# Performance work log

Measured on AMD Instinct MI355X. Metric: run time of the kernel, lower is better.

## Reference

```python
import jax, jax.numpy as jnp
import numpy as np

C = 16          # number of classes
LAM = 25.0      # lambda_param (invariance)
MU = 25.0       # mu_param (variance)
NU = 1.0        # nu_param (covariance)
ALPHA = 50.0    # alpha_param (class-discriminative margin & weight)
EPS = 1e-4


def setup_inputs() -> dict:
    key = jax.random.key(0)
    k1, k2, k3 = jax.random.split(key, 3)
    N, D = 32768, 256
    z_a = jax.random.normal(k1, (N, D), dtype=jnp.float32)
    z_b = jax.random.normal(k2, (N, D), dtype=jnp.float32)
    labels = jax.random.randint(k3, (N,), 0, C)
    return {"z_a": z_a, "z_b": z_b, "labels": labels}


def _class_stats(x, labels):
    # counts [C], mean [C,D], unbiased var [C,D] via one segmented pass
    ones = jnp.ones(x.shape[0], x.dtype)
    counts = jax.ops.segment_sum(ones, labels, num_segments=C)
    s = jax.ops.segment_sum(x, labels, num_segments=C)
    sq = jax.ops.segment_sum(x * x, labels, num_segments=C)
    mean = s / counts[:, None]
    var = (sq - counts[:, None] * mean * mean) / (counts[:, None] - 1.0)
    return counts, mean, var


def _variance_loss(var):
    # mean over classes of mean_D relu(1 - std); D equal per class -> global mean
    std = jnp.sqrt(var + EPS)
    return jnp.mean(jax.nn.relu(1.0 - std))


def _covariance_loss(x, labels, counts, mean):
    D = x.shape[1]
    e = x - mean[labels]  # centered per class

    def per_class(c):
        w = (labels == c).astype(x.dtype)
        em = e * w[:, None]
        cov = em.T @ em / (counts[c] - 1.0)  # [D, D]
        off = (cov * cov).sum() - (jnp.diagonal(cov) ** 2).sum()
        return off / D

    return jnp.mean(jax.lax.map(per_class, jnp.arange(C)))


def _class_disc_loss(mean_a, mean_b):
    m = 0.5 * (mean_a + mean_b)               # [C, D]
    diff = m[:, None, :] - m[None, :, :]      # [C, C, D]
    d2 = jnp.sum(diff * diff, axis=-1)        # [C, C]
    mask = jnp.triu(jnp.ones((C, C), bool), 1)
    dist = jnp.sqrt(jnp.where(mask, d2, 1.0))  # safe sqrt off-mask
    pen = jnp.where(mask, jax.nn.relu(ALPHA - dist) ** 2, 0.0)
    npairs = C * (C - 1) // 2
    return pen.sum() / npairs


def reference(z_a, z_b, labels):
    inv_loss = jnp.mean((z_a - z_b) ** 2)
    ca, ma, va = _class_stats(z_a, labels)
    cb, mb, vb = _class_stats(z_b, labels)
    var_loss = 0.5 * (_variance_loss(va) + _variance_loss(vb))
    cov_loss = 0.5 * (_covariance_loss(z_a, labels, ca, ma)
                      + _covariance_loss(z_b, labels, cb, mb))
    class_loss = _class_disc_loss(ma, mb)
    return LAM * inv_loss + MU * var_loss + NU * cov_loss + ALPHA * class_loss
```

## Files before the change

kernel.cpp:

```cpp
#include <hip/hip_runtime.h>
#include <math.h>

#define N_ROWS 32768
#define D 256
#define C 16

#define WS_SUMS_A 0
#define WS_SQ_A   4096
#define WS_SUMS_B 8192
#define WS_SQ_B   12288
#define WS_INV    16384
#define WS_COV    16385
#define WS_COUNTS 16392
#define WS_CURSOR 16408
#define WS_POFFP  16424
#define WS_EOFF   16448
#define WS_INVP   16512
#define WS_COVP   17024
#define WS_PERM   17920
#define WS_ZERO_FLOATS 16408

#define WS_PSUM   50688
#define WS_HPART  181760
#define WS_GPART2 189952
#define GP_TILE2  4096
#define NTASK     10
#define NSPLIT    8
#define K2        2
#define GP_PER_SPLIT2 (NTASK * C * 2 * GP_TILE2)
#define RIDX_CAP  1024
#define NEED_A ((size_t)(WS_GPART2 + NSPLIT * GP_PER_SPLIT2) * 4)

typedef __attribute__((ext_vector_type(8))) __bf16 bf16x8;
typedef __attribute__((ext_vector_type(16))) float f32x16;

__device__ inline unsigned bf16_rne(float f) {
    unsigned u = __float_as_uint(f);
    return (u + 0x7fffu + ((u >> 16) & 1u)) >> 16;
}
__device__ inline unsigned pack_bf16(float lo, float hi) {
    return bf16_rne(lo) | (bf16_rne(hi) << 16);
}
__device__ inline int img_base4(int c, int kd) {
    return c * 20 + ((kd + ((c >> 1) & 12)) & 12);
}
__device__ inline int img_base2(int c, int kd) {
    return c * 20 + ((kd + ((c >> 1) & 12)) & 14);
}
__device__ inline void task_rc(int w, int& r, int& c) {
    if (w < 4)      { r = 0; c = w; }
    else if (w < 7) { r = 1; c = w - 3; }
    else if (w < 9) { r = 2; c = w - 5; }
    else            { r = 3; c = 3; }
}


__global__ __launch_bounds__(256) void k_pre(const float* __restrict__ za,
                                             const float* __restrict__ zb,
                                             const int* __restrict__ labels,
                                             int* __restrict__ hpart,
                                             float* __restrict__ ws) {
    const int t = threadIdx.x;
    const int b = blockIdx.x;
    __shared__ int h[C];
    if (t < C) h[t] = 0;
    __syncthreads();
    if (t < 64) atomicAdd(&h[labels[b * 64 + t]], 1);

    const int base = b * 4096 + t;
    float acc = 0.f;
    #pragma unroll
    for (int k = 0; k < 16; ++k) {
        const int i = base + k * 256;
        const float4 a = ((const float4*)za)[i];
        const float4 v = ((const float4*)zb)[i];
        const float dx = a.x - v.x, dy = a.y - v.y;
        const float dz = a.z - v.z, dw = a.w - v.w;
        acc += dx * dx + dy * dy + dz * dz + dw * dw;
    }
    for (int o = 32; o > 0; o >>= 1) acc += __shfl_down(acc, o, 64);
    __shared__ float red[4];
    if ((t & 63) == 0) red[t >> 6] = acc;
    __syncthreads();
    if (t < C) hpart[b * C + t] = h[t];
    if (t == 0) ws[WS_INVP + b] = red[0] + red[1] + red[2] + red[3];
}

__global__ __launch_bounds__(512) void k_scatter2(const int* __restrict__ labels,
                                                  const int* __restrict__ hpart,
                                                  int* __restrict__ counts,
                                                  int* __restrict__ poffp,
                                                  int* __restrict__ eoffp,
                                                  int* __restrict__ perm) {
    const int t = threadIdx.x;
    const int B = blockIdx.x;
    __shared__ int lh[C];
    __shared__ int tot[32][C];
    __shared__ int pre[32][C];
    __shared__ int ccnt[C], cpre[C], ceoff[C];
    const int i = B * 512 + t;
    const int lab = labels[i];
    if (t < C) lh[t] = 0;
    const int c = t & 15, seg = t >> 4;
    {
        int tt = 0, pp = 0;
        const int plo = seg * 16, pcut = B * 8;
        #pragma unroll
        for (int p = plo; p < plo + 16; ++p) {
            const int v = hpart[p * C + c];
            tt += v;
            if (p < pcut) pp += v;
        }
        tot[seg][c] = tt;
        pre[seg][c] = pp;
    }
    __syncthreads();
    const int lr = atomicAdd(&lh[lab], 1);
    if (t < C) {
        int s1 = 0, s2 = 0;
        #pragma unroll
        for (int g = 0; g < 32; ++g) { s1 += tot[g][t]; s2 += pre[g][t]; }
        ccnt[t] = s1;
        cpre[t] = s2;
    }
    __syncthreads();
    if (t == 0) {
        int off = 0, po = 0;
        for (int cc = 0; cc < C; ++cc) {
            ceoff[cc] = off;
            if (B == 0) { eoffp[cc] = off; poffp[cc] = po; counts[cc] = ccnt[cc]; }
            off += ccnt[cc];
            po += (ccnt[cc] + 31) >> 5;
        }
        if (B == 0) { eoffp[C] = off; poffp[C] = po; }
    }
    __syncthreads();
    perm[ceoff[lab] + cpre[lab] + lr] = i;
}

__global__ __launch_bounds__(640) void k_gram6(const float* __restrict__ za,
                                               const float* __restrict__ zb,
                                               const int* __restrict__ perm,
                                               const int* __restrict__ counts,
                                               const int* __restrict__ poffp,
                                               const int* __restrict__ eoffp,
                                               float* __restrict__ ws) {
    const int t = threadIdx.x;
    const int split = blockIdx.x;
    const int cls = blockIdx.y, inp = blockIdx.z;
    const float* X = inp ? zb : za;
    const int cnt = counts[cls];
    const int eoff = eoffp[cls];
    const int nsteps = poffp[cls + 1] - poffp[cls];
    const int chunk = (nsteps + NSPLIT - 1) / NSPLIT;
    const int sb = split * chunk;
    const int se = min(sb + chunk, nsteps);

    __shared__ __align__(16) unsigned img[2][5120];
    __shared__ float sstats[512];
    __shared__ int ridx[RIDX_CAP];

    for (int i = t; i < 512; i += 640) sstats[i] = 0.f;
    const int nl = (se > sb) ? (se - sb) * 32 : 0;
    for (int i = t; i < nl && i < RIDX_CAP; i += 640) {
        const int gr = sb * 32 + i;
        ridx[i] = (gr < cnt) ? perm[eoff + gr] : -1;
    }
    __syncthreads();

    auto rowidx = [&](int li) -> int {
        if (li < RIDX_CAP) return ridx[li];
        const int gr = sb * 32 + li;
        return (gr < cnt) ? perm[eoff + gr] : -1;
    };

    const int lane = t & 63, w = t >> 6;
    const int cg = lane & 31, q = lane >> 5;
    int tr, tc;
    task_rc(w, tr, tc);
    const bool stg = (t < 512);

    const int lc = 4 * (t & 63);
    const int kp0 = 2 * ((t >> 6) & 7);

    f32x16 acc[2][2];
    #pragma unroll
    for (int i = 0; i < 2; ++i)
        #pragma unroll
        for (int j = 0; j < 2; ++j) acc[i][j] = 0.0f;

    float s1r[4] = {0.f, 0.f, 0.f, 0.f};
    float s2r[4] = {0.f, 0.f, 0.f, 0.f};
    float4 f0[2], f1[2];

    auto load_regs = [&](int s) {
        #pragma unroll
        for (int it = 0; it < 2; ++it) {
            const int li = (s - sb) * 32 + 2 * (kp0 + it);
            const int r0 = rowidx(li), r1 = rowidx(li + 1);
            f0[it] = (r0 >= 0) ? *(const float4*)(X + (size_t)r0 * D + lc)
                               : make_float4(0.f, 0.f, 0.f, 0.f);
            f1[it] = (r1 >= 0) ? *(const float4*)(X + (size_t)r1 * D + lc)
                               : make_float4(0.f, 0.f, 0.f, 0.f);
        }
    };
    auto pack_store = [&](int buf) {
        unsigned pw[4][2];
        #pragma unroll
        for (int it = 0; it < 2; ++it) {
            pw[0][it] = pack_bf16(f0[it].x, f1[it].x);
            pw[1][it] = pack_bf16(f0[it].y, f1[it].y);
            pw[2][it] = pack_bf16(f0[it].z, f1[it].z);
            pw[3][it] = pack_bf16(f0[it].w, f1[it].w);
        }
        #pragma unroll
        for (int d = 0; d < 4; ++d)
            *(uint2*)&img[buf][img_base2(lc + d, kp0)] = make_uint2(pw[d][0], pw[d][1]);
        #pragma unroll
        for (int it = 0; it < 2; ++it) {
            s1r[0] += f0[it].x + f1[it].x; s2r[0] += f0[it].x * f0[it].x + f1[it].x * f1[it].x;
            s1r[1] += f0[it].y + f1[it].y; s2r[1] += f0[it].y * f0[it].y + f1[it].y * f1[it].y;
            s1r[2] += f0[it].z + f1[it].z; s2r[2] += f0[it].z * f0[it].z + f1[it].z * f1[it].z;
            s1r[3] += f0[it].w + f1[it].w; s2r[3] += f0[it].w * f0[it].w + f1[it].w * f1[it].w;
        }
    };
    auto frag = [&](int buf, int col, int kd) -> bf16x8 {
        return *(const bf16x8*)&img[buf][img_base4(col, kd)];
    };

    if (sb < se) {
        if (stg) { load_regs(sb); pack_store(0); }
        __syncthreads();
        for (int s = sb; s < se; ++s) {
            const int buf = (s - sb) & 1;
            const bool more = (s + 1 < se);
            if (stg && more) load_regs(s + 1);
            #pragma unroll
            for (int h = 0; h < 2; ++h) {
                const int kd = h * 8 + q * 4;
                bf16x8 a0 = frag(buf, tr * 64 + cg, kd);
                bf16x8 a1 = frag(buf, tr * 64 + 32 + cg, kd);
                bf16x8 b0, b1;
                if (tr == tc) { b0 = a0; b1 = a1; }
                else {
                    b0 = frag(buf, tc * 64 + cg, kd);
                    b1 = frag(buf, tc * 64 + 32 + cg, kd);
                }
                acc[0][0] = __builtin_amdgcn_mfma_f32_32x32x16_bf16(a0, b0, acc[0][0], 0, 0, 0);
                acc[0][1] = __builtin_amdgcn_mfma_f32_32x32x16_bf16(a0, b1, acc[0][1], 0, 0, 0);
                acc[1][0] = __builtin_amdgcn_mfma_f32_32x32x16_bf16(a1, b0, acc[1][0], 0, 0, 0);
                acc[1][1] = __builtin_amdgcn_mfma_f32_32x32x16_bf16(a1, b1, acc[1][1], 0, 0, 0);
            }
            if (stg && more) pack_store(buf ^ 1);
            __syncthreads();
        }
    }

    float* gp = ws + WS_GPART2 + (size_t)split * GP_PER_SPLIT2
              + (((size_t)cls * 2 + inp) * NTASK + w) * GP_TILE2;
    #pragma unroll
    for (int i = 0; i < 2; ++i)
        #pragma unroll
        for (int j = 0; j < 2; ++j)
            #pragma unroll
            for (int r = 0; r < 16; ++r) {
                const int row = i * 32 + (r & 3) + 8 * (r >> 2) + 4 * q;
                const int col = j * 32 + cg;
                gp[row * 64 + col] = acc[i][j][r];
            }

    if (stg) {
        #pragma unroll
        for (int d = 0; d < 4; ++d) {
            atomicAdd(&sstats[lc + d],       s1r[d]);
            atomicAdd(&sstats[256 + lc + d], s2r[d]);
        }
    }
    __syncthreads();
    const size_t pbase = (((size_t)split * C + cls) * 2 + inp) * 512;
    for (int i = t; i < 512; i += 640) ws[WS_PSUM + pbase + i] = sstats[i];
}

__global__ __launch_bounds__(256) void k_reduce2(float* __restrict__ ws) {
    const int t = threadIdx.x;
    const int c = blockIdx.x;
    const int stat = blockIdx.y & 1, inp = blockIdx.y >> 1;
    float acc = 0.f;
    #pragma unroll
    for (int sp = 0; sp < NSPLIT; ++sp)
        acc += ws[WS_PSUM + (((size_t)sp * C + c) * 2 + inp) * 512 + stat * 256 + t];
    const int base = stat ? (inp ? WS_SQ_B : WS_SQ_A)
                          : (inp ? WS_SUMS_B : WS_SUMS_A);
    ws[base + c * D + t] = acc;
}

__global__ __launch_bounds__(256) void k_cov2(const int* __restrict__ counts,
                                              float* __restrict__ ws) {
    const int t = threadIdx.x;
    const int w = blockIdx.x / K2, k0 = blockIdx.x % K2;
    int tr, tc;
    task_rc(w, tr, tc);
    const int cls = blockIdx.y, inp = blockIdx.z;
    const int cnt = counts[cls];
    const float fc = (float)cnt;
    const float cinv = 1.f / fc, uinv = 1.f / (fc - 1.f);
    const float wgt = (tr == tc) ? 1.f : 2.f;
    __shared__ float Mr[64], Mc[64];
    const float* sums = ws + (inp ? WS_SUMS_B : WS_SUMS_A) + cls * D;
    if (t < 64) Mr[t] = sums[tr * 64 + t] * cinv;
    else if (t < 128) Mc[t - 64] = sums[tc * 64 + (t - 64)] * cinv;
    __syncthreads();

    const float* gp0 = ws + WS_GPART2 + (((size_t)cls * 2 + inp) * NTASK + w) * GP_TILE2;
    float local = 0.f;
    #pragma unroll
    for (int kk = 0; kk < 2048 / 256; ++kk) {
        const int e = k0 * 2048 + kk * 256 + t;
        float g = 0.f;
        #pragma unroll
        for (int sp = 0; sp < NSPLIT; ++sp)
            g += gp0[(size_t)sp * GP_PER_SPLIT2 + e];
        const int row = e >> 6, col = e & 63;
        const float cov = (g - fc * Mr[row] * Mc[col]) * uinv;
        if (!(tr == tc && row == col)) local += wgt * cov * cov;
    }
    for (int o = 32; o > 0; o >>= 1) local += __shfl_down(local, o, 64);
    __shared__ float red[4];
    if ((t & 63) == 0) red[t >> 6] = local;
    __syncthreads();
    if (t == 0)
        ws[WS_COVP + (((size_t)inp * C + cls) * NTASK + w) * K2 + k0] =
            red[0] + red[1] + red[2] + red[3];
}

__global__ __launch_bounds__(512) void k_hist(const int* __restrict__ labels,
                                              int* __restrict__ counts) {
    __shared__ int h[C];
    const int t = threadIdx.x;
    if (t < C) h[t] = 0;
    __syncthreads();
    const int i = blockIdx.x * 512 + t;
    atomicAdd(&h[labels[i]], 1);
    __syncthreads();
    if (t < C) atomicAdd(&counts[t], h[t]);
}

__global__ void k_scan(const int* __restrict__ counts, int* __restrict__ cursor,
                       int* __restrict__ poffp, int* __restrict__ eoffp) {
    if (threadIdx.x == 0) {
        int off = 0, po = 0;
        for (int c = 0; c < C; ++c) {
            cursor[c] = off;
            eoffp[c] = off;
            poffp[c] = po;
            off += counts[c];
            po += (counts[c] + 31) >> 5;
        }
        poffp[C] = po;
        eoffp[C] = off;
    }
}

__global__ __launch_bounds__(512) void k_scatter(const int* __restrict__ labels,
                                                 int* __restrict__ cursor,
                                                 int* __restrict__ perm) {
    __shared__ int lh[C];
    __shared__ int lbase[C];
    const int t = threadIdx.x;
    if (t < C) lh[t] = 0;
    __syncthreads();
    const int i = blockIdx.x * 512 + t;
    const int lab = labels[i];
    const int lr = atomicAdd(&lh[lab], 1);
    __syncthreads();
    if (t < C) lbase[t] = atomicAdd(&cursor[t], lh[t]);
    __syncthreads();
    perm[lbase[lab] + lr] = i;
}

__global__ __launch_bounds__(256) void k_stats(const float* __restrict__ za,
                                               const float* __restrict__ zb,
                                               const int* __restrict__ labels,
                                               float* __restrict__ ws) {
    const int t = threadIdx.x;
    __shared__ float S[4][C * D];
    __shared__ int lab[512];
    for (int i = t; i < 4 * C * D; i += 256) ((float*)S)[i] = 0.f;
    const int r0 = blockIdx.x * 512;
    for (int i = t; i < 512; i += 256) lab[i] = labels[r0 + i];
    __syncthreads();
    float invp = 0.f;
    #pragma unroll 4
    for (int rr = 0; rr < 512; ++rr) {
        const int l = lab[rr];
        const float a = za[(size_t)(r0 + rr) * D + t];
        const float b = zb[(size_t)(r0 + rr) * D + t];
        const float dd = a - b;
        invp += dd * dd;
        S[0][l * D + t] += a;
        S[1][l * D + t] += a * a;
        S[2][l * D + t] += b;
        S[3][l * D + t] += b * b;
    }
    __syncthreads();
    #pragma unroll
    for (int c = 0; c < C; ++c) {
        atomicAdd(&ws[WS_SUMS_A + c * D + t], S[0][c * D + t]);
        atomicAdd(&ws[WS_SQ_A   + c * D + t], S[1][c * D + t]);
        atomicAdd(&ws[WS_SUMS_B + c * D + t], S[2][c * D + t]);
        atomicAdd(&ws[WS_SQ_B   + c * D + t], S[3][c * D + t]);
    }
    for (int o = 32; o > 0; o >>= 1) invp += __shfl_down(invp, o, 64);
    if ((t & 63) == 0) atomicAdd(&ws[WS_INV], invp);
}

#define STR 20
#define KB 32
__global__ __launch_bounds__(256) void k_gram_slow(const float* __restrict__ za,
                                                   const float* __restrict__ zb,
                                                   const int* __restrict__ perm,
                                                   const int* __restrict__ counts,
                                                   float* __restrict__ ws) {
    const int t = threadIdx.x;
    const int tile = blockIdx.x;
    const int tx = tile >> 1, ty = (tile + 1) >> 1;
    const int cls = blockIdx.y;
    const int inp = blockIdx.z;
    const float* X = inp ? zb : za;
    const float* sums = ws + (inp ? WS_SUMS_B : WS_SUMS_A) + cls * D;
    int offs = 0;
    for (int c = 0; c < cls; ++c) offs += counts[c];
    const int cnt = counts[cls];
    const int cm0 = tx * 128, cn0 = ty * 128;
    __shared__ __align__(16) unsigned lds[2][256 * STR];
    const int p = t >> 5, cq = t & 31;
    const int lane = t & 63, w = t >> 6;
    const int wr = w & 1, wc = w >> 1;
    const int cg = lane & 31, q = lane >> 5;
    f32x16 acc[2][2];
    #pragma unroll
    for (int i = 0; i < 2; ++i)
        #pragma unroll
        for (int j = 0; j < 2; ++j) acc[i][j] = 0.0f;
    const int nsteps = (cnt + KB - 1) / KB;
    auto stage = [&](int buf, int k0) {
        #pragma unroll
        for (int ch = 0; ch < 2; ++ch) {
            const int gc = (ch ? cn0 : cm0) + 4 * cq;
            #pragma unroll
            for (int sub = 0; sub < 2; ++sub) {
                const int rr = sub * 16 + 2 * p;
                const int r0 = k0 + rr, r1 = r0 + 1;
                float4 v0 = make_float4(0.f, 0.f, 0.f, 0.f), v1 = v0;
                if (r0 < cnt) v0 = *(const float4*)(X + (size_t)perm[offs + r0] * D + gc);
                if (r1 < cnt) v1 = *(const float4*)(X + (size_t)perm[offs + r1] * D + gc);
                unsigned* dst = &lds[buf][(ch * 128 + 4 * cq) * STR + (rr >> 1)];
                dst[0 * STR] = pack_bf16(v0.x, v1.x);
                dst[1 * STR] = pack_bf16(v0.y, v1.y);
                dst[2 * STR] = pack_bf16(v0.z, v1.z);
                dst[3 * STR] = pack_bf16(v0.w, v1.w);
            }
        }
    };
    auto frag = [&](int buf, int colbase, int h) -> bf16x8 {
        return *(const bf16x8*)&lds[buf][(colbase + cg) * STR + h * 8 + q * 4];
    };
    stage(0, 0);
    for (int s = 0; s < nsteps; ++s) {
        __syncthreads();
        const int buf = s & 1;
        if (s + 1 < nsteps) stage(buf ^ 1, (s + 1) * KB);
        #pragma unroll
        for (int h = 0; h < 2; ++h) {
            bf16x8 a0 = frag(buf, wr * 64, h);
            bf16x8 a1 = frag(buf, wr * 64 + 32, h);
            bf16x8 b0 = frag(buf, 128 + wc * 64, h);
            bf16x8 b1 = frag(buf, 128 + wc * 64 + 32, h);
            acc[0][0] = __builtin_amdgcn_mfma_f32_32x32x16_bf16(a0, b0, acc[0][0], 0, 0, 0);
            acc[0][1] = __builtin_amdgcn_mfma_f32_32x32x16_bf16(a0, b1, acc[0][1], 0, 0, 0);
            acc[1][0] = __builtin_amdgcn_mfma_f32_32x32x16_bf16(a1, b0, acc[1][0], 0, 0, 0);
            acc[1][1] = __builtin_amdgcn_mfma_f32_32x32x16_bf16(a1, b1, acc[1][1], 0, 0, 0);
        }
    }
    const float fc = (float)cnt;
    const float cinv = 1.f / fc, uinv = 1.f / (fc - 1.f);
    const float wgt = (tx == ty) ? 1.f : 2.f;
    float local = 0.f;
    #pragma unroll
    for (int i = 0; i < 2; ++i) {
        #pragma unroll
        for (int j = 0; j < 2; ++j) {
            const int gn = cn0 + wc * 64 + j * 32 + (lane & 31);
            const float mn = sums[gn] * cinv;
            #pragma unroll
            for (int r = 0; r < 16; ++r) {
                const int row = (r & 3) + 8 * (r >> 2) + 4 * q;
                const int gm = cm0 + wr * 64 + i * 32 + row;
                const float cov = (acc[i][j][r] - fc * (sums[gm] * cinv) * mn) * uinv;
                if (gm != gn) local += wgt * cov * cov;
            }
        }
    }
    for (int o = 32; o > 0; o >>= 1) local += __shfl_down(local, o, 64);
    if (lane == 0) atomicAdd(&ws[WS_COV], local);
}

__global__ __launch_bounds__(256) void k_final(const float* __restrict__ ws,
                                               float* __restrict__ out,
                                               int fast) {
    __shared__ float M[C * D];
    __shared__ float redv[4], redi[4], redc[4], redp[4];
    const int t = threadIdx.x;
    const int* counts = (const int*)ws + WS_COUNTS;

    float vsum = 0.f;
    for (int idx = t; idx < 2 * C * D; idx += 256) {
        const int inp = idx >> 12;
        const int cd = idx & 4095;
        const int c = cd >> 8;
        const float cnt = (float)counts[c];
        const float s  = ws[(inp ? WS_SUMS_B : WS_SUMS_A) + cd];
        const float sq = ws[(inp ? WS_SQ_B   : WS_SQ_A)   + cd];
        const float mean = s / cnt;
        const float var = (sq - cnt * mean * mean) / (cnt - 1.f);
        vsum += fmaxf(1.f - sqrtf(var + 1e-4f), 0.f);
    }
    float isum, csum;
    if (fast) {
        isum = ws[WS_INVP + t] + ws[WS_INVP + 256 + t];
        csum = ws[WS_COVP + t] + ws[WS_COVP + 256 + t]
             + ((t < 128) ? ws[WS_COVP + 512 + t] : 0.f);
    } else {
        isum = (t == 0) ? ws[WS_INV] : 0.f;
        csum = (t == 0) ? ws[WS_COV] : 0.f;
    }
    for (int cd = t; cd < C * D; cd += 256) {
        const int c = cd >> 8;
        const float cnt = (float)counts[c];
        M[cd] = 0.5f * (ws[WS_SUMS_A + cd] + ws[WS_SUMS_B + cd]) / cnt;
    }
    for (int o = 32; o > 0; o >>= 1) {
        vsum += __shfl_down(vsum, o, 64);
        isum += __shfl_down(isum, o, 64);
        csum += __shfl_down(csum, o, 64);
    }
    if ((t & 63) == 0) {
        redv[t >> 6] = vsum; redi[t >> 6] = isum; redc[t >> 6] = csum;
    }
    __syncthreads();

    const int wv = t >> 6, ln = t & 63;
    float psum = 0.f;
    int p = 0;
    for (int i = 0; i < C; ++i) {
        for (int j = i + 1; j < C; ++j, ++p) {
            if ((p & 3) != wv) continue;
            float d2 = 0.f;
            #pragma unroll
            for (int d = ln; d < D; d += 64) {
                const float df = M[i * D + d] - M[j * D + d];
                d2 += df * df;
            }
            for (int o = 32; o > 0; o >>= 1) d2 += __shfl_down(d2, o, 64);
            if (ln == 0) {
                const float dist = sqrtf(d2);
                const float r = fmaxf(50.f - dist, 0.f);
                psum += r * r;
            }
        }
    }
    if (ln == 0) redp[wv] = psum;
    __syncthreads();

    if (t == 0) {
        const float var_loss = (redv[0] + redv[1] + redv[2] + redv[3]) / 8192.f;
        const float class_loss = (redp[0] + redp[1] + redp[2] + redp[3]) / 120.f;
        const float inv_loss = (redi[0] + redi[1] + redi[2] + redi[3]) / (float)(N_ROWS * D);
        const float cov_loss = 0.5f * (redc[0] + redc[1] + redc[2] + redc[3]) / (float)(C * D);
        out[0] = 25.f * inv_loss + 25.f * var_loss + 1.f * cov_loss + 50.f * class_loss;
    }
}

extern "C" void kernel_launch(void* const* d_in, const int* in_sizes, int n_in,
                              void* d_out, int out_size, void* d_ws, size_t ws_size,
                              hipStream_t stream) {
    const float* za = (const float*)d_in[0];
    const float* zb = (const float*)d_in[1];
    const int* labels = (const int*)d_in[2];
    float* out = (float*)d_out;
    float* ws = (float*)d_ws;
    int* wsi = (int*)d_ws;

    if (ws_size >= NEED_A) {
        k_pre<<<512, 256, 0, stream>>>(za, zb, labels, wsi + WS_HPART, ws);
        k_scatter2<<<64, 512, 0, stream>>>(labels, wsi + WS_HPART, wsi + WS_COUNTS,
                                           wsi + WS_POFFP, wsi + WS_EOFF, wsi + WS_PERM);
        k_gram6<<<dim3(NSPLIT, C, 2), 640, 0, stream>>>(
            za, zb, wsi + WS_PERM, wsi + WS_COUNTS, wsi + WS_POFFP,
            wsi + WS_EOFF, ws);
        k_reduce2<<<dim3(C, 4), 256, 0, stream>>>(ws);
        k_cov2<<<dim3(NTASK * K2, C, 2), 256, 0, stream>>>(wsi + WS_COUNTS, ws);
        k_final<<<1, 256, 0, stream>>>(ws, out, 1);
    } else {
        hipMemsetAsync(d_ws, 0, WS_ZERO_FLOATS * sizeof(float), stream);
        k_hist<<<64, 512, 0, stream>>>(labels, wsi + WS_COUNTS);
        k_scan<<<1, 64, 0, stream>>>(wsi + WS_COUNTS, wsi + WS_CURSOR,
                                     wsi + WS_POFFP, wsi + WS_EOFF);
        k_scatter<<<64, 512, 0, stream>>>(labels, wsi + WS_CURSOR, wsi + WS_PERM);
        k_stats<<<64, 256, 0, stream>>>(za, zb, labels, ws);
        k_gram_slow<<<dim3(3, C, 2), 256, 0, stream>>>(za, zb, wsi + WS_PERM,
                                                       wsi + WS_COUNTS, ws);
        k_final<<<1, 256, 0, stream>>>(ws, out, 0);
    }
}
```

Baseline: 161.7 us.

## Fuse stats reduce, covariance, and final loss into one kernel with bf16 partials

Removes the separate k_reduce2 and k_final launches. Their work moves into a single k_cov3 kernel: each block reduces the per-split sums it needs, block w==0 writes the class sums, and the last block (found with an atomic counter) computes the final loss. The per-split Gram partial tiles are now stored as packed bf16 pairs instead of fp32, which halves the partial-buffer traffic between the Gram and covariance kernels. The trade-off is extra precision loss in the covariance partial sums, a serialized tail on the last block, and reliance on threadfence ordering for correctness.

```diff
diff --git a/kernel.cpp b/kernel.cpp
--- a/kernel.cpp
+++ b/kernel.cpp
@@ -11,6 +11,7 @@
 #define WS_SQ_B   12288
 #define WS_INV    16384
 #define WS_COV    16385
+#define WS_CTR    16386
 #define WS_COUNTS 16392
 #define WS_CURSOR 16408
 #define WS_POFFP  16424
@@ -23,13 +24,12 @@
 #define WS_PSUM   50688
 #define WS_HPART  181760
 #define WS_GPART2 189952
-#define GP_TILE2  4096
+#define GP_TILE2P 2048
 #define NTASK     10
 #define NSPLIT    8
-#define K2        2
-#define GP_PER_SPLIT2 (NTASK * C * 2 * GP_TILE2)
+#define GP_PER_SPLIT2P (NTASK * C * 2 * GP_TILE2P)
 #define RIDX_CAP  1024
-#define NEED_A ((size_t)(WS_GPART2 + NSPLIT * GP_PER_SPLIT2) * 4)
+#define NEED_A ((size_t)(WS_GPART2 + NSPLIT * GP_PER_SPLIT2P) * 4)
 
 typedef __attribute__((ext_vector_type(8))) __bf16 bf16x8;
 typedef __attribute__((ext_vector_type(16))) float f32x16;
@@ -66,6 +66,7 @@
     if (t < C) h[t] = 0;
     __syncthreads();
     if (t < 64) atomicAdd(&h[labels[b * 64 + t]], 1);
+    if (b == 0 && t == 0) ((int*)ws)[WS_CTR] = 0;
 
     const int base = b * 4096 + t;
     float acc = 0.f;
@@ -256,18 +257,15 @@
         }
     }
 
-    float* gp = ws + WS_GPART2 + (size_t)split * GP_PER_SPLIT2
-              + (((size_t)cls * 2 + inp) * NTASK + w) * GP_TILE2;
+    unsigned* gp = (unsigned*)ws + WS_GPART2 + (size_t)split * GP_PER_SPLIT2P
+                 + (((size_t)cls * 2 + inp) * NTASK + w) * GP_TILE2P;
     #pragma unroll
     for (int i = 0; i < 2; ++i)
         #pragma unroll
-        for (int j = 0; j < 2; ++j)
-            #pragma unroll
-            for (int r = 0; r < 16; ++r) {
-                const int row = i * 32 + (r & 3) + 8 * (r >> 2) + 4 * q;
-                const int col = j * 32 + cg;
-                gp[row * 64 + col] = acc[i][j][r];
-            }
+        for (int r = 0; r < 16; ++r) {
+            const int row = i * 32 + (r & 3) + 8 * (r >> 2) + 4 * q;
+            gp[row * 32 + cg] = pack_bf16(acc[i][0][r], acc[i][1][r]);
+        }
 
     if (stg) {
         #pragma unroll
@@ -281,23 +279,11 @@
     for (int i = t; i < 512; i += 640) ws[WS_PSUM + pbase + i] = sstats[i];
 }
 
-__global__ __launch_bounds__(256) void k_reduce2(float* __restrict__ ws) {
-    const int t = threadIdx.x;
-    const int c = blockIdx.x;
-    const int stat = blockIdx.y & 1, inp = blockIdx.y >> 1;
-    float acc = 0.f;
-    #pragma unroll
-    for (int sp = 0; sp < NSPLIT; ++sp)
-        acc += ws[WS_PSUM + (((size_t)sp * C + c) * 2 + inp) * 512 + stat * 256 + t];
-    const int base = stat ? (inp ? WS_SQ_B : WS_SQ_A)
-                          : (inp ? WS_SUMS_B : WS_SUMS_A);
-    ws[base + c * D + t] = acc;
-}
-
-__global__ __launch_bounds__(256) void k_cov2(const int* __restrict__ counts,
-                                              float* __restrict__ ws) {
-    const int t = threadIdx.x;
-    const int w = blockIdx.x / K2, k0 = blockIdx.x % K2;
+__global__ __launch_bounds__(256) void k_cov3(const int* __restrict__ counts,
+                                              float* __restrict__ ws,
+                                              float* __restrict__ out) {
+    const int t = threadIdx.x;
+    const int w = blockIdx.x;
     int tr, tc;
     task_rc(w, tr, tc);
     const int cls = blockIdx.y, inp = blockIdx.z;
@@ -306,31 +292,133 @@
     const float cinv = 1.f / fc, uinv = 1.f / (fc - 1.f);
     const float wgt = (tr == tc) ? 1.f : 2.f;
     __shared__ float Mr[64], Mc[64];
-    const float* sums = ws + (inp ? WS_SUMS_B : WS_SUMS_A) + cls * D;
-    if (t < 64) Mr[t] = sums[tr * 64 + t] * cinv;
-    else if (t < 128) Mc[t - 64] = sums[tc * 64 + (t - 64)] * cinv;
-    __syncthreads();
-
-    const float* gp0 = ws + WS_GPART2 + (((size_t)cls * 2 + inp) * NTASK + w) * GP_TILE2;
+    if (t < 64) {
+        float s = 0.f;
+        #pragma unroll
+        for (int sp = 0; sp < NSPLIT; ++sp)
+            s += ws[WS_PSUM + (((size_t)sp * C + cls) * 2 + inp) * 512 + tr * 64 + t];
+        Mr[t] = s * cinv;
+    } else if (t < 128) {
+        const int u = t - 64;
+        float s = 0.f;
+        #pragma unroll
+        for (int sp = 0; sp < NSPLIT; ++sp)
+            s += ws[WS_PSUM + (((size_t)sp * C + cls) * 2 + inp) * 512 + tc * 64 + u];
+        Mc[u] = s * cinv;
+    }
+    if (w == 0) {
+        float s1 = 0.f, s2 = 0.f;
+        #pragma unroll
+        for (int sp = 0; sp < NSPLIT; ++sp) {
+            const size_t pb = WS_PSUM + (((size_t)sp * C + cls) * 2 + inp) * 512;
+            s1 += ws[pb + t];
+            s2 += ws[pb + 256 + t];
+        }
+        ws[(inp ? WS_SUMS_B : WS_SUMS_A) + cls * D + t] = s1;
+        ws[(inp ? WS_SQ_B   : WS_SQ_A)   + cls * D + t] = s2;
+    }
+    __syncthreads();
+
+    const unsigned* gp0 = (const unsigned*)ws + WS_GPART2
+                        + (((size_t)cls * 2 + inp) * NTASK + w) * GP_TILE2P;
     float local = 0.f;
     #pragma unroll
-    for (int kk = 0; kk < 2048 / 256; ++kk) {
-        const int e = k0 * 2048 + kk * 256 + t;
-        float g = 0.f;
-        #pragma unroll
-        for (int sp = 0; sp < NSPLIT; ++sp)
-            g += gp0[(size_t)sp * GP_PER_SPLIT2 + e];
-        const int row = e >> 6, col = e & 63;
-        const float cov = (g - fc * Mr[row] * Mc[col]) * uinv;
-        if (!(tr == tc && row == col)) local += wgt * cov * cov;
+    for (int kk = 0; kk < GP_TILE2P / 256; ++kk) {
+        const int e = kk * 256 + t;
+        float glo = 0.f, ghi = 0.f;
+        #pragma unroll
+        for (int sp = 0; sp < NSPLIT; ++sp) {
+            const unsigned u = gp0[(size_t)sp * GP_PER_SPLIT2P + e];
+            glo += __uint_as_float(u << 16);
+            ghi += __uint_as_float(u & 0xffff0000u);
+        }
+        const int row = e >> 5, c0 = e & 31;
+        const float mr = Mr[row];
+        const float clo = (glo - fc * mr * Mc[c0]) * uinv;
+        const float chi = (ghi - fc * mr * Mc[c0 + 32]) * uinv;
+        if (!(tr == tc && row == c0))      local += wgt * clo * clo;
+        if (!(tr == tc && row == c0 + 32)) local += wgt * chi * chi;
     }
     for (int o = 32; o > 0; o >>= 1) local += __shfl_down(local, o, 64);
     __shared__ float red[4];
     if ((t & 63) == 0) red[t >> 6] = local;
     __syncthreads();
     if (t == 0)
-        ws[WS_COVP + (((size_t)inp * C + cls) * NTASK + w) * K2 + k0] =
+        ws[WS_COVP + ((size_t)inp * C + cls) * NTASK + w] =
             red[0] + red[1] + red[2] + red[3];
+
+    __shared__ int isLast;
+    __threadfence();
+    __syncthreads();
+    if (t == 0) {
+        const int old = atomicAdd((int*)ws + WS_CTR, 1);
+        isLast = (old == NTASK * C * 2 - 1);
+    }
+    __syncthreads();
+    if (!isLast) return;
+    __threadfence();
+
+    __shared__ float M[C * D];
+    __shared__ float redv[4], redi[4], redc[4], redp[4];
+    float vsum = 0.f;
+    for (int idx = t; idx < 2 * C * D; idx += 256) {
+        const int ip = idx >> 12;
+        const int cd = idx & 4095;
+        const int cc = cd >> 8;
+        const float cn = (float)counts[cc];
+        const float s  = ws[(ip ? WS_SUMS_B : WS_SUMS_A) + cd];
+        const float sq = ws[(ip ? WS_SQ_B   : WS_SQ_A)   + cd];
+        const float mean = s / cn;
+        const float var = (sq - cn * mean * mean) / (cn - 1.f);
+        vsum += fmaxf(1.f - sqrtf(var + 1e-4f), 0.f);
+    }
+    float isum = ws[WS_INVP + t] + ws[WS_INVP + 256 + t];
+    float csum = ws[WS_COVP + t] + ((t < 64) ? ws[WS_COVP + 256 + t] : 0.f);
+    for (int cd = t; cd < C * D; cd += 256) {
+        const int cc = cd >> 8;
+        const float cn = (float)counts[cc];
+        M[cd] = 0.5f * (ws[WS_SUMS_A + cd] + ws[WS_SUMS_B + cd]) / cn;
+    }
+    for (int o = 32; o > 0; o >>= 1) {
+        vsum += __shfl_down(vsum, o, 64);
+        isum += __shfl_down(isum, o, 64);
+        csum += __shfl_down(csum, o, 64);
+    }
+    if ((t & 63) == 0) {
+        redv[t >> 6] = vsum; redi[t >> 6] = isum; redc[t >> 6] = csum;
+    }
+    __syncthreads();
+
+    const int wv = t >> 6, ln = t & 63;
+    float psum = 0.f;
+    int p = 0;
+    for (int i = 0; i < C; ++i) {
+        for (int j = i + 1; j < C; ++j, ++p) {
+            if ((p & 3) != wv) continue;
+            float d2 = 0.f;
+            #pragma unroll
+            for (int d = ln; d < D; d += 64) {
+                const float df = M[i * D + d] - M[j * D + d];
+                d2 += df * df;
+            }
+            for (int o = 32; o > 0; o >>= 1) d2 += __shfl_down(d2, o, 64);
+            if (ln == 0) {
+                const float dist = sqrtf(d2);
+                const float r = fmaxf(50.f - dist, 0.f);
+                psum += r * r;
+            }
+        }
+    }
+    if (ln == 0) redp[wv] = psum;
+    __syncthreads();
+
+    if (t == 0) {
+        const float var_loss = (redv[0] + redv[1] + redv[2] + redv[3]) / 8192.f;
+        const float class_loss = (redp[0] + redp[1] + redp[2] + redp[3]) / 120.f;
+        const float inv_loss = (redi[0] + redi[1] + redi[2] + redi[3]) / (float)(N_ROWS * D);
+        const float cov_loss = 0.5f * (redc[0] + redc[1] + redc[2] + redc[3]) / (float)(C * D);
+        out[0] = 25.f * inv_loss + 25.f * var_loss + 1.f * cov_loss + 50.f * class_loss;
+    }
 }
 
 __global__ __launch_bounds__(512) void k_hist(const int* __restrict__ labels,
@@ -506,8 +594,7 @@
 }
 
 __global__ __launch_bounds__(256) void k_final(const float* __restrict__ ws,
-                                               float* __restrict__ out,
-                                               int fast) {
+                                               float* __restrict__ out) {
     __shared__ float M[C * D];
     __shared__ float redv[4], redi[4], redc[4], redp[4];
     const int t = threadIdx.x;
@@ -525,15 +612,8 @@
         const float var = (sq - cnt * mean * mean) / (cnt - 1.f);
         vsum += fmaxf(1.f - sqrtf(var + 1e-4f), 0.f);
     }
-    float isum, csum;
-    if (fast) {
-        isum = ws[WS_INVP + t] + ws[WS_INVP + 256 + t];
-        csum = ws[WS_COVP + t] + ws[WS_COVP + 256 + t]
-             + ((t < 128) ? ws[WS_COVP + 512 + t] : 0.f);
-    } else {
-        isum = (t == 0) ? ws[WS_INV] : 0.f;
-        csum = (t == 0) ? ws[WS_COV] : 0.f;
-    }
+    float isum = (t == 0) ? ws[WS_INV] : 0.f;
+    float csum = (t == 0) ? ws[WS_COV] : 0.f;
     for (int cd = t; cd < C * D; cd += 256) {
         const int c = cd >> 8;
         const float cnt = (float)counts[c];
@@ -598,9 +678,7 @@
         k_gram6<<<dim3(NSPLIT, C, 2), 640, 0, stream>>>(
             za, zb, wsi + WS_PERM, wsi + WS_COUNTS, wsi + WS_POFFP,
             wsi + WS_EOFF, ws);
-        k_reduce2<<<dim3(C, 4), 256, 0, stream>>>(ws);
-        k_cov2<<<dim3(NTASK * K2, C, 2), 256, 0, stream>>>(wsi + WS_COUNTS, ws);
-        k_final<<<1, 256, 0, stream>>>(ws, out, 1);
+        k_cov3<<<dim3(NTASK, C, 2), 256, 0, stream>>>(wsi + WS_COUNTS, ws, out);
     } else {
         hipMemsetAsync(d_ws, 0, WS_ZERO_FLOATS * sizeof(float), stream);
         k_hist<<<64, 512, 0, stream>>>(labels, wsi + WS_COUNTS);
@@ -610,6 +688,6 @@
         k_stats<<<64, 256, 0, stream>>>(za, zb, labels, ws);
         k_gram_slow<<<dim3(3, C, 2), 256, 0, stream>>>(za, zb, wsi + WS_PERM,
                                                        wsi + WS_COUNTS, ws);
-        k_final<<<1, 256, 0, stream>>>(ws, out, 0);
-    }
-}
+        k_final<<<1, 256, 0, stream>>>(ws, out);
+    }
+}
```

Measured after the change: 176.1 us. 1.09x slower.

## Store Gram partials as packed bf16 and fold stat reduction into covariance kernel

Applied to the files above, without the earlier changes.

The Gram kernel now writes its per-split partial tiles as bf16 pairs packed into 32-bit words, halving partial-buffer traffic. The covariance kernel reads them with vectorized uint4 loads, unpacks and sums them, and also reduces the per-split class sums itself. One block per class/input writes the global sums and squares, which removes the separate k_reduce2 launch. The cost is bf16 rounding of partial Gram values before the split reduction, which adds error to the covariance loss.

```diff
diff --git a/kernel.cpp b/kernel.cpp
--- a/kernel.cpp
+++ b/kernel.cpp
@@ -23,13 +23,13 @@
 #define WS_PSUM   50688
 #define WS_HPART  181760
 #define WS_GPART2 189952
-#define GP_TILE2  4096
+#define GP_TILE2P 2048
 #define NTASK     10
 #define NSPLIT    8
-#define K2        2
-#define GP_PER_SPLIT2 (NTASK * C * 2 * GP_TILE2)
+#define KC        2
+#define GP_PER_SPLIT2P (NTASK * C * 2 * GP_TILE2P)
 #define RIDX_CAP  1024
-#define NEED_A ((size_t)(WS_GPART2 + NSPLIT * GP_PER_SPLIT2) * 4)
+#define NEED_A ((size_t)(WS_GPART2 + NSPLIT * GP_PER_SPLIT2P) * 4)
 
 typedef __attribute__((ext_vector_type(8))) __bf16 bf16x8;
 typedef __attribute__((ext_vector_type(16))) float f32x16;
@@ -256,18 +256,15 @@
         }
     }
 
-    float* gp = ws + WS_GPART2 + (size_t)split * GP_PER_SPLIT2
-              + (((size_t)cls * 2 + inp) * NTASK + w) * GP_TILE2;
+    unsigned* gp = (unsigned*)ws + WS_GPART2 + (size_t)split * GP_PER_SPLIT2P
+                 + (((size_t)cls * 2 + inp) * NTASK + w) * GP_TILE2P;
     #pragma unroll
     for (int i = 0; i < 2; ++i)
         #pragma unroll
-        for (int j = 0; j < 2; ++j)
-            #pragma unroll
-            for (int r = 0; r < 16; ++r) {
-                const int row = i * 32 + (r & 3) + 8 * (r >> 2) + 4 * q;
-                const int col = j * 32 + cg;
-                gp[row * 64 + col] = acc[i][j][r];
-            }
+        for (int r = 0; r < 16; ++r) {
+            const int row = i * 32 + (r & 3) + 8 * (r >> 2) + 4 * q;
+            gp[row * 32 + cg] = pack_bf16(acc[i][0][r], acc[i][1][r]);
+        }
 
     if (stg) {
         #pragma unroll
@@ -281,23 +278,10 @@
     for (int i = t; i < 512; i += 640) ws[WS_PSUM + pbase + i] = sstats[i];
 }
 
-__global__ __launch_bounds__(256) void k_reduce2(float* __restrict__ ws) {
-    const int t = threadIdx.x;
-    const int c = blockIdx.x;
-    const int stat = blockIdx.y & 1, inp = blockIdx.y >> 1;
-    float acc = 0.f;
-    #pragma unroll
-    for (int sp = 0; sp < NSPLIT; ++sp)
-        acc += ws[WS_PSUM + (((size_t)sp * C + c) * 2 + inp) * 512 + stat * 256 + t];
-    const int base = stat ? (inp ? WS_SQ_B : WS_SQ_A)
-                          : (inp ? WS_SUMS_B : WS_SUMS_A);
-    ws[base + c * D + t] = acc;
-}
-
-__global__ __launch_bounds__(256) void k_cov2(const int* __restrict__ counts,
+__global__ __launch_bounds__(256) void k_cov4(const int* __restrict__ counts,
                                               float* __restrict__ ws) {
     const int t = threadIdx.x;
-    const int w = blockIdx.x / K2, k0 = blockIdx.x % K2;
+    const int w = blockIdx.x / KC, k0 = blockIdx.x % KC;
     int tr, tc;
     task_rc(w, tr, tc);
     const int cls = blockIdx.y, inp = blockIdx.z;
@@ -306,30 +290,68 @@
     const float cinv = 1.f / fc, uinv = 1.f / (fc - 1.f);
     const float wgt = (tr == tc) ? 1.f : 2.f;
     __shared__ float Mr[64], Mc[64];
-    const float* sums = ws + (inp ? WS_SUMS_B : WS_SUMS_A) + cls * D;
-    if (t < 64) Mr[t] = sums[tr * 64 + t] * cinv;
-    else if (t < 128) Mc[t - 64] = sums[tc * 64 + (t - 64)] * cinv;
-    __syncthreads();
-
-    const float* gp0 = ws + WS_GPART2 + (((size_t)cls * 2 + inp) * NTASK + w) * GP_TILE2;
+    if (t < 64) {
+        float s = 0.f;
+        #pragma unroll
+        for (int sp = 0; sp < NSPLIT; ++sp)
+            s += ws[WS_PSUM + (((size_t)sp * C + cls) * 2 + inp) * 512 + tr * 64 + t];
+        Mr[t] = s * cinv;
+    } else if (t < 128) {
+        const int u = t - 64;
+        float s = 0.f;
+        #pragma unroll
+        for (int sp = 0; sp < NSPLIT; ++sp)
+            s += ws[WS_PSUM + (((size_t)sp * C + cls) * 2 + inp) * 512 + tc * 64 + u];
+        Mc[u] = s * cinv;
+    }
+    if (w == 0 && k0 == 0) {
+        float s1 = 0.f, s2 = 0.f;
+        #pragma unroll
+        for (int sp = 0; sp < NSPLIT; ++sp) {
+            const size_t pb = WS_PSUM + (((size_t)sp * C + cls) * 2 + inp) * 512;
+            s1 += ws[pb + t];
+            s2 += ws[pb + 256 + t];
+        }
+        ws[(inp ? WS_SUMS_B : WS_SUMS_A) + cls * D + t] = s1;
+        ws[(inp ? WS_SQ_B   : WS_SQ_A)   + cls * D + t] = s2;
+    }
+    __syncthreads();
+
+    const int e0 = k0 * 1024 + t * 4;
+    const unsigned* gp0 = (const unsigned*)ws + WS_GPART2
+                        + (((size_t)cls * 2 + inp) * NTASK + w) * GP_TILE2P + e0;
+    uint4 u4[NSPLIT];
+    #pragma unroll
+    for (int sp = 0; sp < NSPLIT; ++sp)
+        u4[sp] = *(const uint4*)(gp0 + (size_t)sp * GP_PER_SPLIT2P);
+
+    float glo[4] = {0.f, 0.f, 0.f, 0.f};
+    float ghi[4] = {0.f, 0.f, 0.f, 0.f};
+    #pragma unroll
+    for (int sp = 0; sp < NSPLIT; ++sp) {
+        const unsigned* uu = (const unsigned*)&u4[sp];
+        #pragma unroll
+        for (int j = 0; j < 4; ++j) {
+            glo[j] += __uint_as_float(uu[j] << 16);
+            ghi[j] += __uint_as_float(uu[j] & 0xffff0000u);
+        }
+    }
+    const int row = e0 >> 5, c0 = e0 & 31;
+    const float mr = Mr[row];
     float local = 0.f;
     #pragma unroll
-    for (int kk = 0; kk < 2048 / 256; ++kk) {
-        const int e = k0 * 2048 + kk * 256 + t;
-        float g = 0.f;
-        #pragma unroll
-        for (int sp = 0; sp < NSPLIT; ++sp)
-            g += gp0[(size_t)sp * GP_PER_SPLIT2 + e];
-        const int row = e >> 6, col = e & 63;
-        const float cov = (g - fc * Mr[row] * Mc[col]) * uinv;
-        if (!(tr == tc && row == col)) local += wgt * cov * cov;
+    for (int j = 0; j < 4; ++j) {
+        const float clo = (glo[j] - fc * mr * Mc[c0 + j]) * uinv;
+        const float chi = (ghi[j] - fc * mr * Mc[c0 + j + 32]) * uinv;
+        if (!(tr == tc && row == c0 + j))      local += wgt * clo * clo;
+        if (!(tr == tc && row == c0 + j + 32)) local += wgt * chi * chi;
     }
     for (int o = 32; o > 0; o >>= 1) local += __shfl_down(local, o, 64);
     __shared__ float red[4];
     if ((t & 63) == 0) red[t >> 6] = local;
     __syncthreads();
     if (t == 0)
-        ws[WS_COVP + (((size_t)inp * C + cls) * NTASK + w) * K2 + k0] =
+        ws[WS_COVP + (((size_t)inp * C + cls) * NTASK + w) * KC + k0] =
             red[0] + red[1] + red[2] + red[3];
 }
 
@@ -598,8 +620,7 @@
         k_gram6<<<dim3(NSPLIT, C, 2), 640, 0, stream>>>(
             za, zb, wsi + WS_PERM, wsi + WS_COUNTS, wsi + WS_POFFP,
             wsi + WS_EOFF, ws);
-        k_reduce2<<<dim3(C, 4), 256, 0, stream>>>(ws);
-        k_cov2<<<dim3(NTASK * K2, C, 2), 256, 0, stream>>>(wsi + WS_COUNTS, ws);
+        k_cov4<<<dim3(NTASK * KC, C, 2), 256, 0, stream>>>(wsi + WS_COUNTS, ws);
         k_final<<<1, 256, 0, stream>>>(ws, out, 1);
     } else {
         hipMemsetAsync(d_ws, 0, WS_ZERO_FLOATS * sizeof(float), stream);
```

After: 159.5 us. About the same (-1.4%).
